# Kernel tuning notes

Measured on AMD Instinct MI355X. Metric: run time of the kernel, lower is better.

The kernel has to match this reference:

```python
import math
import jax, jax.numpy as jnp
import numpy as np

N_HEAD = 16
N_STATE = 1024
N_CTX = 2048
BATCH = 4


def setup_inputs() -> dict:
    key = jax.random.key(0)
    ks = jax.random.split(key, 5)
    s = 1.0 / math.sqrt(N_STATE)
    x = jax.random.normal(ks[0], (BATCH, N_CTX, N_STATE), dtype=jnp.float32)
    # Linear weights stored as [in, out] (y = x @ W + b), equivalent math to torch nn.Linear
    w_attn = jax.random.normal(ks[1], (N_STATE, 3 * N_STATE), dtype=jnp.float32) * s
    b_attn = jax.random.normal(ks[2], (3 * N_STATE,), dtype=jnp.float32) * 0.02
    w_proj = jax.random.normal(ks[3], (N_STATE, N_STATE), dtype=jnp.float32) * s
    b_proj = jax.random.normal(ks[4], (N_STATE,), dtype=jnp.float32) * 0.02
    return {"x": x, "w_attn": w_attn, "b_attn": b_attn, "w_proj": w_proj, "b_proj": b_proj}


def reference(x, w_attn, b_attn, w_proj, b_proj):
    B, T, C = x.shape
    H = N_HEAD
    D = C // H  # d_head
    qkv = x @ w_attn + b_attn                      # [B, T, 3C]
    q, k, v = jnp.split(qkv, 3, axis=2)
    q = q.reshape(B, T, H, D).transpose(0, 2, 1, 3)  # [B, H, T, D]
    k = k.reshape(B, T, H, D).transpose(0, 2, 1, 3)
    v = v.reshape(B, T, H, D).transpose(0, 2, 1, 3)
    scale = 1.0 / math.sqrt(D)
    qk = jnp.einsum('bhqd,bhkd->bhqk', q, k) * scale  # [B, H, T, T]
    causal = jnp.tril(jnp.ones((T, T), dtype=bool))
    qk = jnp.where(causal[None, None], qk, jnp.finfo(qk.dtype).min)
    att = jax.nn.softmax(qk, axis=-1)
    out = jnp.einsum('bhqk,bhkd->bhqd', att, v)      # [B, H, T, D]
    out = out.transpose(0, 2, 1, 3).reshape(B, T, C)
    return out @ w_proj + b_proj
```

## Files before the change

kernel.cpp:

```cpp
#include <hip/hip_runtime.h>
#include <hip/hip_bf16.h>
#include <math.h>

typedef __bf16 bf16;
typedef __bf16 bf16x8 __attribute__((ext_vector_type(8)));
typedef __bf16 bf16x4 __attribute__((ext_vector_type(4)));
typedef __bf16 bf16x2 __attribute__((ext_vector_type(2)));
typedef float f32x4 __attribute__((ext_vector_type(4)));
typedef float f32x16 __attribute__((ext_vector_type(16)));
typedef int int4v __attribute__((ext_vector_type(4)));

static constexpr int B_ = 4, T_ = 2048, C_ = 1024, H_ = 16, D_ = 64;
static constexpr int M_ = B_ * T_;
static constexpr int NQKV = 3 * C_;
static constexpr int K_ = C_;

__device__ __forceinline__ bf16 to_bf16(float f) { return (bf16)f; }

__device__ __forceinline__ void gload_lds16(const void* g, void* l) {
  __builtin_amdgcn_global_load_lds(
      (const __attribute__((address_space(1))) void*)g,
      (__attribute__((address_space(3))) void*)l, 16, 0, 0);
}

__global__ void cvt_x_kernel(const float* __restrict__ in, bf16* __restrict__ out) {
  int i = (blockIdx.x * blockDim.x + threadIdx.x) * 4;
  float4 v = *reinterpret_cast<const float4*>(in + i);
  bf16x4 o;
  o[0] = to_bf16(v.x); o[1] = to_bf16(v.y); o[2] = to_bf16(v.z); o[3] = to_bf16(v.w);
  *reinterpret_cast<bf16x4*>(out + i) = o;
}

__global__ void transpose_cvt_kernel(const float* __restrict__ in, bf16* __restrict__ out,
                                     int ROWS, int COLS) {
  __shared__ float tile[32][33];
  int c0 = blockIdx.x * 32, r0 = blockIdx.y * 32;
  int tx = threadIdx.x, ty = threadIdx.y;
#pragma unroll
  for (int i = 0; i < 32; i += 8)
    tile[ty + i][tx] = in[(size_t)(r0 + ty + i) * COLS + c0 + tx];
  __syncthreads();
#pragma unroll
  for (int i = 0; i < 32; i += 8)
    out[(size_t)(c0 + ty + i) * ROWS + r0 + tx] = to_bf16(tile[tx][ty + i]);
}

template <bool QKV>
__global__ __launch_bounds__(256) void gemm_kernel(
    const bf16* __restrict__ A, const bf16* __restrict__ Bt,
    const float* __restrict__ bias,
    bf16* __restrict__ qo, bf16* __restrict__ ko, bf16* __restrict__ vo,
    float* __restrict__ co) {
  __shared__ bf16 As[128 * 64];
  __shared__ bf16 Bs[128 * 64];
  const int bm = blockIdx.x, bn = blockIdx.y;
  const int tid = threadIdx.x;
  const int lane = tid & 63, wave = tid >> 6;
  const int wm = wave >> 1, wn = wave & 1;
  const int l15 = lane & 15, lg = lane >> 4;
  const int l3 = lane >> 3, l7 = lane & 7;
  const int sslot = l7 ^ l3;

  const bf16* asrc[4];
  const bf16* bsrc[4];
#pragma unroll
  for (int j = 0; j < 4; ++j) {
    const int row = wave * 32 + j * 8 + l3;
    asrc[j] = A + (size_t)(bm * 128 + row) * K_ + sslot * 8;
    bsrc[j] = Bt + (size_t)(bn * 128 + row) * K_ + sslot * 8;
  }

  f32x4 acc[4][4] = {};

  for (int k0 = 0; k0 < K_; k0 += 64) {
#pragma unroll
    for (int j = 0; j < 4; ++j) {
      gload_lds16(asrc[j] + k0, &As[(wave * 32 + j * 8) * 64]);
      gload_lds16(bsrc[j] + k0, &Bs[(wave * 32 + j * 8) * 64]);
    }
    __syncthreads();
    bf16x8 af[4][2], bf[4][2];
#pragma unroll
    for (int m = 0; m < 4; ++m)
#pragma unroll
      for (int kk = 0; kk < 2; ++kk)
        af[m][kk] = *reinterpret_cast<const bf16x8*>(
            &As[(wm * 64 + m * 16 + l15) * 64 + (((kk * 4 + lg) ^ (l15 & 7)) * 8)]);
#pragma unroll
    for (int n = 0; n < 4; ++n)
#pragma unroll
      for (int kk = 0; kk < 2; ++kk)
        bf[n][kk] = *reinterpret_cast<const bf16x8*>(
            &Bs[(wn * 64 + n * 16 + l15) * 64 + (((kk * 4 + lg) ^ (l15 & 7)) * 8)]);
#pragma unroll
    for (int kk = 0; kk < 2; ++kk)
#pragma unroll
      for (int m = 0; m < 4; ++m)
#pragma unroll
        for (int n = 0; n < 4; ++n)
          acc[m][n] =
              __builtin_amdgcn_mfma_f32_16x16x32_bf16(af[m][kk], bf[n][kk], acc[m][n], 0, 0, 0);
    __syncthreads();
  }

  const int colbase = bn * 128 + wn * 64;
  const int rowbase = bm * 128 + wm * 64;
  if (QKV) {
    const int sec = (bn * 128) >> 10;
#pragma unroll
    for (int n = 0; n < 4; ++n) {
      const int col = colbase + n * 16 + l15;
      const float bv = bias[col];
      const int cc = col & 1023;
      const int h = cc >> 6, d = cc & 63;
#pragma unroll
      for (int m = 0; m < 4; ++m) {
        const int row0 = rowbase + m * 16 + lg * 4;
        const int b = row0 >> 11, t0 = row0 & 2047;
        if (sec == 2) {
          bf16x4 pv;
#pragma unroll
          for (int r = 0; r < 4; ++r) pv[r] = to_bf16(acc[m][n][r] + bv);
          *reinterpret_cast<bf16x4*>(&vo[((size_t)(b * 16 + h) * 64 + d) * 2048 + t0]) = pv;
        } else if (sec == 0) {
#pragma unroll
          for (int r = 0; r < 4; ++r)
            qo[((size_t)(b * 16 + h) * 2048 + t0 + r) * 64 + d] =
                to_bf16((acc[m][n][r] + bv) * 0.125f);
        } else {
#pragma unroll
          for (int r = 0; r < 4; ++r)
            ko[((size_t)(b * 16 + h) * 2048 + t0 + r) * 64 + d] = to_bf16(acc[m][n][r] + bv);
        }
      }
    }
  } else {
#pragma unroll
    for (int n = 0; n < 4; ++n) {
      const int col = colbase + n * 16 + l15;
      const float bv = bias[col];
#pragma unroll
      for (int m = 0; m < 4; ++m) {
#pragma unroll
        for (int r = 0; r < 4; ++r) {
          const int row = rowbase + m * 16 + lg * 4 + r;
          co[(size_t)row * 1024 + col] = acc[m][n][r] + bv;
        }
      }
    }
  }
}

__device__ __forceinline__ int pack_bf2(float lo, float hi) {
  bf16x2 t; t[0] = (bf16)lo; t[1] = (bf16)hi;
  return __builtin_bit_cast(int, t);
}

template <int R0>
__device__ __forceinline__ bf16x8 pack_pstep(f32x16 pf, int h) {
  int a  = pack_bf2(pf[R0 + 0], pf[R0 + 1]);
  int b2 = pack_bf2(pf[R0 + 2], pf[R0 + 3]);
  int c  = pack_bf2(pf[R0 + 4], pf[R0 + 5]);
  int d2 = pack_bf2(pf[R0 + 6], pf[R0 + 7]);
  int pa = __shfl_xor(a, 32);
  int pb = __shfl_xor(b2, 32);
  int pc = __shfl_xor(c, 32);
  int pd = __shfl_xor(d2, 32);
  int4v pi = {h ? pc : a, h ? pd : b2, h ? c : pa, h ? d2 : pb};
  return __builtin_bit_cast(bf16x8, pi);
}

__global__ __launch_bounds__(256) void attn_kernel(
    const bf16* __restrict__ q, const bf16* __restrict__ k,
    const bf16* __restrict__ vT, bf16* __restrict__ o) {
  const int bid = blockIdx.x;
  const int xcd = bid & 7;
  const int local = bid >> 3;
  const int qt = 15 - (local >> 3);
  const int bh = xcd * 8 + (local & 7);
  const int tid = threadIdx.x;
  const int lane = tid & 63, w = tid >> 6;
  const int l31 = lane & 31, hi = lane >> 5;
  const char* qp = (const char*)(q + (size_t)bh * T_ * D_);
  const char* kp = (const char*)(k + (size_t)bh * T_ * D_);
  const char* vp = (const char*)(vT + (size_t)bh * D_ * T_);
  const int lofKQ = l31 * 128 + hi * 16;
  const int lofV  = l31 * 4096 + hi * 16;
  const int bb = bh >> 4, hh = bh & 15;
  bf16* obase = o + (size_t)bb * T_ * C_ + hh * 64;

  const int qrow0 = qt * 128 + w * 32;
  const int qg = qrow0 + l31;

  bf16x8 qf[4];
#pragma unroll
  for (int s = 0; s < 4; ++s)
    qf[s] = *reinterpret_cast<const bf16x8*>(qp + (size_t)qrow0 * 128 + s * 32 + lofKQ);

  f32x16 ot0 = {}, ot1 = {};
  float mrun = -INFINITY, lrun = 0.f;

  for (int tb = 0; tb < qrow0 + 32; tb += 64) {
    f32x16 st0 = {}, st1 = {};
#pragma unroll
    for (int s = 0; s < 4; ++s) {
      bf16x8 k0 = *reinterpret_cast<const bf16x8*>(kp + (size_t)tb * 128 + s * 32 + lofKQ);
      bf16x8 k1 = *reinterpret_cast<const bf16x8*>(kp + (size_t)(tb + 32) * 128 + s * 32 + lofKQ);
      st0 = __builtin_amdgcn_mfma_f32_32x32x16_bf16(k0, qf[s], st0, 0, 0, 0);
      st1 = __builtin_amdgcn_mfma_f32_32x32x16_bf16(k1, qf[s], st1, 0, 0, 0);
    }
    bf16x8 va[2][4];
#pragma unroll
    for (int dt = 0; dt < 2; ++dt)
#pragma unroll
      for (int s = 0; s < 4; ++s)
        va[dt][s] = *reinterpret_cast<const bf16x8*>(
            vp + (size_t)dt * 32 * 4096 + (size_t)(tb + s * 16) * 2 + lofV);
    if (tb + 63 > qrow0) {
#pragma unroll
      for (int r = 0; r < 16; ++r) {
        const int koff = (r & 3) + 8 * (r >> 2) + 4 * hi;
        if (tb + koff > qg) st0[r] = -1e30f;
        if (tb + 32 + koff > qg) st1[r] = -1e30f;
      }
    }
    float mx[16];
#pragma unroll
    for (int r = 0; r < 16; ++r) mx[r] = fmaxf(st0[r], st1[r]);
#pragma unroll
    for (int d = 8; d > 0; d >>= 1)
#pragma unroll
      for (int r = 0; r < d; ++r) mx[r] = fmaxf(mx[r], mx[r + d]);
    const float pmax = fmaxf(mx[0], __shfl_xor(mx[0], 32));
    if (__any(pmax > mrun + 8.f)) {
      const float mnew = fmaxf(mrun, pmax);
      const float corr = __expf(mrun - mnew);
      lrun *= corr;
#pragma unroll
      for (int r = 0; r < 16; ++r) { ot0[r] *= corr; ot1[r] *= corr; }
      mrun = mnew;
    }
#pragma unroll
    for (int r = 0; r < 16; ++r) {
      st0[r] = __expf(st0[r] - mrun);
      st1[r] = __expf(st1[r] - mrun);
    }
    float sm[16];
#pragma unroll
    for (int r = 0; r < 16; ++r) sm[r] = st0[r] + st1[r];
#pragma unroll
    for (int d = 8; d > 0; d >>= 1)
#pragma unroll
      for (int r = 0; r < d; ++r) sm[r] += sm[r + d];
    lrun += sm[0] + __shfl_xor(sm[0], 32);
    bf16x8 pb[4];
    pb[0] = pack_pstep<0>(st0, hi);
    pb[1] = pack_pstep<8>(st0, hi);
    pb[2] = pack_pstep<0>(st1, hi);
    pb[3] = pack_pstep<8>(st1, hi);
#pragma unroll
    for (int s = 0; s < 4; ++s) {
      ot0 = __builtin_amdgcn_mfma_f32_32x32x16_bf16(va[0][s], pb[s], ot0, 0, 0, 0);
      ot1 = __builtin_amdgcn_mfma_f32_32x32x16_bf16(va[1][s], pb[s], ot1, 0, 0, 0);
    }
  }

  const float inv = 1.f / lrun;
  bf16* orow = obase + (size_t)qg * C_;
#pragma unroll
  for (int dt = 0; dt < 2; ++dt) {
#pragma unroll
    for (int rg = 0; rg < 4; ++rg) {
      bf16x4 pv;
#pragma unroll
      for (int j = 0; j < 4; ++j)
        pv[j] = to_bf16(((dt ? ot1 : ot0)[rg * 4 + j]) * inv);
      *reinterpret_cast<bf16x4*>(orow + dt * 32 + rg * 8 + 4 * hi) = pv;
    }
  }
}

extern "C" void kernel_launch(void* const* d_in, const int* in_sizes, int n_in,
                              void* d_out, int out_size, void* d_ws, size_t ws_size,
                              hipStream_t stream) {
  const float* x      = (const float*)d_in[0];
  const float* w_attn = (const float*)d_in[1];
  const float* b_attn = (const float*)d_in[2];
  const float* w_proj = (const float*)d_in[3];
  const float* b_proj = (const float*)d_in[4];
  float* out = (float*)d_out;

  char* ws = (char*)d_ws;
  size_t off = 0;
  bf16* xb  = (bf16*)(ws + off); off += (size_t)M_ * K_ * 2;
  bf16* wta = (bf16*)(ws + off); off += (size_t)NQKV * K_ * 2;
  bf16* wtp = (bf16*)(ws + off); off += (size_t)C_ * K_ * 2;
  bf16* qb  = (bf16*)(ws + off); off += (size_t)M_ * C_ * 2;
  bf16* kb  = (bf16*)(ws + off); off += (size_t)M_ * C_ * 2;
  bf16* vtb = (bf16*)(ws + off); off += (size_t)M_ * C_ * 2;
  bf16* attn_out = xb;

  cvt_x_kernel<<<(M_ * K_) / (4 * 256), 256, 0, stream>>>(x, xb);
  transpose_cvt_kernel<<<dim3(NQKV / 32, K_ / 32), dim3(32, 8), 0, stream>>>(w_attn, wta, K_, NQKV);
  transpose_cvt_kernel<<<dim3(C_ / 32, K_ / 32), dim3(32, 8), 0, stream>>>(w_proj, wtp, K_, C_);
  gemm_kernel<true><<<dim3(M_ / 128, NQKV / 128), 256, 0, stream>>>(
      xb, wta, b_attn, qb, kb, vtb, nullptr);
  attn_kernel<<<1024, 256, 0, stream>>>(qb, kb, vtb, attn_out);
  gemm_kernel<false><<<dim3(M_ / 128, C_ / 128), 256, 0, stream>>>(
      attn_out, wtp, b_proj, nullptr, nullptr, nullptr, out);
}
```

Before: 308.0 us.

## Stage K/V tiles through double-buffered swizzled LDS in attention kernel

The attention kernel now loads each 64-key K and V^T tile cooperatively into shared memory using direct global-to-LDS loads, double-buffered so the next tile is fetched while the current one is computed. Before this, each wave read K and V from global memory separately. The shared tiles are shared across the 4 waves of a block and XOR-swizzled to avoid LDS bank conflicts. The cost is a block-wide barrier every iteration, and waves whose causal range ends early now sit idle while the others finish.

```diff
diff --git a/kernel.cpp b/kernel.cpp
--- a/kernel.cpp
+++ b/kernel.cpp
@@ -173,6 +173,8 @@
 __global__ __launch_bounds__(256) void attn_kernel(
     const bf16* __restrict__ q, const bf16* __restrict__ k,
     const bf16* __restrict__ vT, bf16* __restrict__ o) {
+  __shared__ bf16 Ks[2][64 * 64];
+  __shared__ bf16 Vs[2][64 * 64];
   const int bid = blockIdx.x;
   const int xcd = bid & 7;
   const int local = bid >> 3;
@@ -181,16 +183,19 @@
   const int tid = threadIdx.x;
   const int lane = tid & 63, w = tid >> 6;
   const int l31 = lane & 31, hi = lane >> 5;
+  const int l8r = lane >> 3, l8c = lane & 7;
+  const int soff = (l8c * 16) ^ ((l8r & 7) << 4);
+  const int rsw = (l31 & 7) << 4;
   const char* qp = (const char*)(q + (size_t)bh * T_ * D_);
   const char* kp = (const char*)(k + (size_t)bh * T_ * D_);
   const char* vp = (const char*)(vT + (size_t)bh * D_ * T_);
   const int lofKQ = l31 * 128 + hi * 16;
-  const int lofV  = l31 * 4096 + hi * 16;
   const int bb = bh >> 4, hh = bh & 15;
   bf16* obase = o + (size_t)bb * T_ * C_ + hh * 64;
 
   const int qrow0 = qt * 128 + w * 32;
   const int qg = qrow0 + l31;
+  const int nt = 2 * qt + 2;
 
   bf16x8 qf[4];
 #pragma unroll
@@ -200,69 +205,91 @@
   f32x16 ot0 = {}, ot1 = {};
   float mrun = -INFINITY, lrun = 0.f;
 
-  for (int tb = 0; tb < qrow0 + 32; tb += 64) {
-    f32x16 st0 = {}, st1 = {};
-#pragma unroll
-    for (int s = 0; s < 4; ++s) {
-      bf16x8 k0 = *reinterpret_cast<const bf16x8*>(kp + (size_t)tb * 128 + s * 32 + lofKQ);
-      bf16x8 k1 = *reinterpret_cast<const bf16x8*>(kp + (size_t)(tb + 32) * 128 + s * 32 + lofKQ);
-      st0 = __builtin_amdgcn_mfma_f32_32x32x16_bf16(k0, qf[s], st0, 0, 0, 0);
-      st1 = __builtin_amdgcn_mfma_f32_32x32x16_bf16(k1, qf[s], st1, 0, 0, 0);
-    }
-    bf16x8 va[2][4];
-#pragma unroll
-    for (int dt = 0; dt < 2; ++dt)
-#pragma unroll
-      for (int s = 0; s < 4; ++s)
-        va[dt][s] = *reinterpret_cast<const bf16x8*>(
-            vp + (size_t)dt * 32 * 4096 + (size_t)(tb + s * 16) * 2 + lofV);
-    if (tb + 63 > qrow0) {
+  auto STAGE = [&](int t, int buf) {
+    const int tb = t * 64;
+#pragma unroll
+    for (int j = 0; j < 2; ++j) {
+      const int c = w * 2 + j;
+      gload_lds16(kp + (size_t)(tb + c * 8 + l8r) * 128 + soff, &Ks[buf][c * 8 * 64]);
+      gload_lds16(vp + (size_t)(c * 8 + l8r) * 4096 + (size_t)tb * 2 + soff, &Vs[buf][c * 8 * 64]);
+    }
+  };
+
+  STAGE(0, 0);
+  __syncthreads();
+
+  for (int t = 0; t < nt; ++t) {
+    const int tb = t * 64;
+    const int buf = t & 1;
+    if (t + 1 < nt) STAGE(t + 1, buf ^ 1);
+    if (tb < qrow0 + 32) {
+      const char* kb = (const char*)&Ks[buf][0];
+      const char* vb = (const char*)&Vs[buf][0];
+      f32x16 st0 = {}, st1 = {};
+#pragma unroll
+      for (int s = 0; s < 4; ++s) {
+        bf16x8 k0 = *reinterpret_cast<const bf16x8*>(kb + l31 * 128 + ((s * 32 + hi * 16) ^ rsw));
+        bf16x8 k1 =
+            *reinterpret_cast<const bf16x8*>(kb + (32 + l31) * 128 + ((s * 32 + hi * 16) ^ rsw));
+        st0 = __builtin_amdgcn_mfma_f32_32x32x16_bf16(k0, qf[s], st0, 0, 0, 0);
+        st1 = __builtin_amdgcn_mfma_f32_32x32x16_bf16(k1, qf[s], st1, 0, 0, 0);
+      }
+      bf16x8 va[2][4];
+#pragma unroll
+      for (int dt = 0; dt < 2; ++dt)
+#pragma unroll
+        for (int s = 0; s < 4; ++s)
+          va[dt][s] = *reinterpret_cast<const bf16x8*>(
+              vb + (dt * 32 + l31) * 128 + ((s * 32 + hi * 16) ^ rsw));
+      if (tb + 63 > qrow0) {
+#pragma unroll
+        for (int r = 0; r < 16; ++r) {
+          const int koff = (r & 3) + 8 * (r >> 2) + 4 * hi;
+          if (tb + koff > qg) st0[r] = -1e30f;
+          if (tb + 32 + koff > qg) st1[r] = -1e30f;
+        }
+      }
+      float mx[16];
+#pragma unroll
+      for (int r = 0; r < 16; ++r) mx[r] = fmaxf(st0[r], st1[r]);
+#pragma unroll
+      for (int d = 8; d > 0; d >>= 1)
+#pragma unroll
+        for (int r = 0; r < d; ++r) mx[r] = fmaxf(mx[r], mx[r + d]);
+      const float pmax = fmaxf(mx[0], __shfl_xor(mx[0], 32));
+      if (__any(pmax > mrun + 8.f)) {
+        const float mnew = fmaxf(mrun, pmax);
+        const float corr = __expf(mrun - mnew);
+        lrun *= corr;
+#pragma unroll
+        for (int r = 0; r < 16; ++r) { ot0[r] *= corr; ot1[r] *= corr; }
+        mrun = mnew;
+      }
 #pragma unroll
       for (int r = 0; r < 16; ++r) {
-        const int koff = (r & 3) + 8 * (r >> 2) + 4 * hi;
-        if (tb + koff > qg) st0[r] = -1e30f;
-        if (tb + 32 + koff > qg) st1[r] = -1e30f;
-      }
-    }
-    float mx[16];
-#pragma unroll
-    for (int r = 0; r < 16; ++r) mx[r] = fmaxf(st0[r], st1[r]);
-#pragma unroll
-    for (int d = 8; d > 0; d >>= 1)
-#pragma unroll
-      for (int r = 0; r < d; ++r) mx[r] = fmaxf(mx[r], mx[r + d]);
-    const float pmax = fmaxf(mx[0], __shfl_xor(mx[0], 32));
-    if (__any(pmax > mrun + 8.f)) {
-      const float mnew = fmaxf(mrun, pmax);
-      const float corr = __expf(mrun - mnew);
-      lrun *= corr;
-#pragma unroll
-      for (int r = 0; r < 16; ++r) { ot0[r] *= corr; ot1[r] *= corr; }
-      mrun = mnew;
-    }
-#pragma unroll
-    for (int r = 0; r < 16; ++r) {
-      st0[r] = __expf(st0[r] - mrun);
-      st1[r] = __expf(st1[r] - mrun);
-    }
-    float sm[16];
-#pragma unroll
-    for (int r = 0; r < 16; ++r) sm[r] = st0[r] + st1[r];
-#pragma unroll
-    for (int d = 8; d > 0; d >>= 1)
-#pragma unroll
-      for (int r = 0; r < d; ++r) sm[r] += sm[r + d];
-    lrun += sm[0] + __shfl_xor(sm[0], 32);
-    bf16x8 pb[4];
-    pb[0] = pack_pstep<0>(st0, hi);
-    pb[1] = pack_pstep<8>(st0, hi);
-    pb[2] = pack_pstep<0>(st1, hi);
-    pb[3] = pack_pstep<8>(st1, hi);
-#pragma unroll
-    for (int s = 0; s < 4; ++s) {
-      ot0 = __builtin_amdgcn_mfma_f32_32x32x16_bf16(va[0][s], pb[s], ot0, 0, 0, 0);
-      ot1 = __builtin_amdgcn_mfma_f32_32x32x16_bf16(va[1][s], pb[s], ot1, 0, 0, 0);
-    }
+        st0[r] = __expf(st0[r] - mrun);
+        st1[r] = __expf(st1[r] - mrun);
+      }
+      float sm[16];
+#pragma unroll
+      for (int r = 0; r < 16; ++r) sm[r] = st0[r] + st1[r];
+#pragma unroll
+      for (int d = 8; d > 0; d >>= 1)
+#pragma unroll
+        for (int r = 0; r < d; ++r) sm[r] += sm[r + d];
+      lrun += sm[0] + __shfl_xor(sm[0], 32);
+      bf16x8 pb[4];
+      pb[0] = pack_pstep<0>(st0, hi);
+      pb[1] = pack_pstep<8>(st0, hi);
+      pb[2] = pack_pstep<0>(st1, hi);
+      pb[3] = pack_pstep<8>(st1, hi);
+#pragma unroll
+      for (int s = 0; s < 4; ++s) {
+        ot0 = __builtin_amdgcn_mfma_f32_32x32x16_bf16(va[0][s], pb[s], ot0, 0, 0, 0);
+        ot1 = __builtin_amdgcn_mfma_f32_32x32x16_bf16(va[1][s], pb[s], ot1, 0, 0, 0);
+      }
+    }
+    __syncthreads();
   }
 
   const float inv = 1.f / lrun;
```

New measurement: 258.2 us. -16.2%, faster.
